# Optimization experiments

Hardware: AMD Instinct MI355X
Metric: run time of the kernel (lower is better)

The kernel has to match this reference:

```python
import jax, jax.numpy as jnp
import numpy as np

# Flattened-state gather indices. State is prev[9,3] flattened to 27 values,
# then concat with x -> flat[29], where flat[27]=a=x[0], flat[28]=b=x[1].
# Row t gives the (x0, x1, x2) inputs of triangle t, read from the source wiring.
IDX0 = np.array([3, 0, 6, 12, 9, 15, 18, 6, 15])   # x0 inputs
IDX1 = np.array([1, 7, 4, 19, 16, 13, 10, 22, 25])  # x1 inputs
IDX2 = np.array([17, 5, 11, 8, 28, 2, 27, 23, 26])  # x2 inputs (t=4 -> b, t=6 -> a)

NOISE_SCALE = 0.125  # LUT2 hard-codes noise = 0.125


def mux(s, a, b):
    return 0.5 * (s * b - s * a + a + b)


def setup_inputs() -> dict:
    key = jax.random.key(0)
    k1, k2, k3 = jax.random.split(key, 3)
    x = jax.random.normal(k1, (2,), dtype=jnp.float32)
    weights = jax.random.normal(k2, (9, 3, 4), dtype=jnp.float32)  # 9 triangles x 3 LUT2s x 4 weights
    noise = jax.random.normal(k3, (130, 9, 3, 4), dtype=jnp.float32)  # per-step np.random.normal draws
    return {"x": x, "weights": weights, "noise": noise, "dummy1": 0, "dummy2": 0}


def reference(x, weights, noise, dummy1, dummy2):
    del dummy1, dummy2  # unused in the original forward

    def step(prev, n):
        # prev: [9,3] current states; n: [9,3,4] noise for this step
        flat = jnp.concatenate([prev.reshape(-1), x])  # [29]
        x0, x1, x2 = flat[IDX0], flat[IDX1], flat[IDX2]  # each [9]
        # LUT j of each triangle: LUT0(x1,x2), LUT1(x0,x2), LUT2(x0,x1)
        A = jnp.stack([x1, x0, x0], axis=1)  # [9,3] first mux select
        B = jnp.stack([x2, x2, x1], axis=1)  # [9,3] second mux select
        w = weights + jnp.abs(1.0 - jnp.abs(weights)) * n * NOISE_SCALE  # [9,3,4]
        m0 = mux(A, w[..., 0], w[..., 1])
        m1 = mux(A, w[..., 2], w[..., 3])
        new = mux(B, m0, m1)  # [9,3] synchronous update (uupdate after all forwards)
        return new, None

    init = -jnp.ones((9, 3), dtype=x.dtype)  # all states start at -1
    final, _ = jax.lax.scan(step, init, noise)  # 130 steps
    return jnp.stack([final[0, 1], final[1, 2], final[7, 2]])
```

## Files before the change

### kernel.cpp

```cpp
#include <hip/hip_runtime.h>


#define STEPS 130
#define NLUT  27

__device__ __constant__ int c_idx0[9] = {3, 0, 6, 12, 9, 15, 18, 6, 15};
__device__ __constant__ int c_idx1[9] = {1, 7, 4, 19, 16, 13, 10, 22, 25};
__device__ __constant__ int c_idx2[9] = {17, 5, 11, 8, 28, 2, 27, 23, 26};

__global__ __launch_bounds__(1024)
void one_layer_net_kernel(const float* __restrict__ x,
                          const float* __restrict__ weights,
                          const float* __restrict__ noise,
                          float* __restrict__ out) {
    __shared__ float4 tbl[STEPS * NLUT];

    const int tid = threadIdx.x;
    const float a = x[0];
    const float b = x[1];

    const float4* __restrict__ w4 = (const float4*)weights;
    const float4* __restrict__ n4 = (const float4*)noise;
    for (int i = tid; i < STEPS * NLUT; i += 1024) {
        const int l = i % NLUT;
        float4 w = w4[l];
        float4 n = n4[i];
        float w0 = fmaf(fabsf(1.0f - fabsf(w.x)) * n.x, 0.125f, w.x);
        float w1 = fmaf(fabsf(1.0f - fabsf(w.y)) * n.y, 0.125f, w.y);
        float w2 = fmaf(fabsf(1.0f - fabsf(w.z)) * n.z, 0.125f, w.z);
        float w3 = fmaf(fabsf(1.0f - fabsf(w.w)) * n.w, 0.125f, w.w);
        float d0 = w1 - w0, s0 = w0 + w1;
        float d1 = w3 - w2, s1 = w2 + w3;
        float K3 = 0.25f * (d1 - d0);
        float K2 = 0.25f * (s1 - s0);
        float K1 = 0.25f * (d0 + d1);
        float K0 = 0.25f * (s0 + s1);
        if (l == 12 || l == 13) {
            K0 = fmaf(K2, b, K0); K1 = fmaf(K3, b, K1); K2 = 0.0f; K3 = 0.0f;
        }
        if (l == 18 || l == 19) {
            K0 = fmaf(K2, a, K0); K1 = fmaf(K3, a, K1); K2 = 0.0f; K3 = 0.0f;
        }
        tbl[i] = make_float4(K3, K2, K1, K0);
    }
    __syncthreads();

    if (tid >= 64) return;

    const int l  = tid;
    const int lc = (l < NLUT) ? l : (NLUT - 1);
    const int t  = lc / 3;
    const int j  = lc % 3;
    int srcA = (j == 0) ? c_idx1[t] : c_idx0[t];
    int srcB = (j == 2) ? c_idx1[t] : c_idx2[t];
    if (srcB >= NLUT) srcB = 0;
    const int bpA = srcA << 2;
    const int bpB = srcB << 2;

    float state = -1.0f;

    const float4* __restrict__ row = &tbl[lc];
    float4 k = row[0];
    #pragma unroll
    for (int s = 0; s < STEPS; ++s) {
        const float4 kc = k;
        if (s + 1 < STEPS) k = row[(s + 1) * NLUT];
        const int si = __float_as_int(state);
        const float gA = __int_as_float(__builtin_amdgcn_ds_bpermute(bpA, si));
        const float gB = __int_as_float(__builtin_amdgcn_ds_bpermute(bpB, si));
        const float t0 = fmaf(gA, kc.x, kc.y);
        const float t1 = fmaf(gA, kc.z, kc.w);
        state = fmaf(gB, t0, t1);
    }

    if (l == 1)  out[0] = state;
    if (l == 5)  out[1] = state;
    if (l == 23) out[2] = state;
}

extern "C" void kernel_launch(void* const* d_in, const int* in_sizes, int n_in,
                              void* d_out, int out_size, void* d_ws, size_t ws_size,
                              hipStream_t stream) {
    const float* x       = (const float*)d_in[0];
    const float* weights = (const float*)d_in[1];
    const float* noise   = (const float*)d_in[2];
    float* out = (float*)d_out;
    one_layer_net_kernel<<<1, 1024, 0, stream>>>(x, weights, noise, out);
}
```

Before: 65.37 us.

## Unroll recurrence three steps per round via composed wiring to cut bpermute latency chain

Replaces the per-step pair of cross-lane permutes with a three-step composed evaluation: each lane gathers 8 states from three hops back in the wiring graph and evaluates a tree of 7 LUT polynomials, advancing 3 steps per round (43 rounds plus one final step). This shortens the serial dependency chain of ds_bpermute latencies from 130 to 44 rounds. In exchange each round does 8 permutes and 7 LDS table loads plus redundant arithmetic. Correctness depends on the composed wiring and row offsets (steps 3r..3r+2) lining up, and on the clamped srcB=0 path for external inputs being harmless.

```diff
diff --git a/kernel.cpp b/kernel.cpp
--- a/kernel.cpp
+++ b/kernel.cpp
@@ -3,10 +3,29 @@
 
 #define STEPS 130
 #define NLUT  27
+#define ROUNDS 43
 
 __device__ __constant__ int c_idx0[9] = {3, 0, 6, 12, 9, 15, 18, 6, 15};
 __device__ __constant__ int c_idx1[9] = {1, 7, 4, 19, 16, 13, 10, 22, 25};
 __device__ __constant__ int c_idx2[9] = {17, 5, 11, 8, 28, 2, 27, 23, 26};
+
+__device__ __forceinline__ int wA(int m) {
+    int t = m / 3, j = m % 3;
+    return (j == 0) ? c_idx1[t] : c_idx0[t];
+}
+__device__ __forceinline__ int wB(int m) {
+    int t = m / 3, j = m % 3;
+    int s = (j == 2) ? c_idx1[t] : c_idx2[t];
+    return (s >= NLUT) ? 0 : s;
+}
+
+__device__ __forceinline__ float evalE(float4 k, float x, float y) {
+    return fmaf(y, fmaf(x, k.x, k.y), fmaf(x, k.z, k.w));
+}
+
+__device__ __forceinline__ float bperm(int byteIdx, float v) {
+    return __int_as_float(__builtin_amdgcn_ds_bpermute(byteIdx, __float_as_int(v)));
+}
 
 __global__ __launch_bounds__(1024)
 void one_layer_net_kernel(const float* __restrict__ x,
@@ -49,28 +68,53 @@
 
     const int l  = tid;
     const int lc = (l < NLUT) ? l : (NLUT - 1);
-    const int t  = lc / 3;
-    const int j  = lc % 3;
-    int srcA = (j == 0) ? c_idx1[t] : c_idx0[t];
-    int srcB = (j == 2) ? c_idx1[t] : c_idx2[t];
-    if (srcB >= NLUT) srcB = 0;
-    const int bpA = srcA << 2;
-    const int bpB = srcB << 2;
+
+    const int a0 = wA(lc), b0 = wB(lc);
+    const int a1 = wA(a0), b1 = wB(a0);
+    const int a2 = wA(b0), b2 = wB(b0);
+    const int g0 = wA(a1) << 2, g1 = wB(a1) << 2;
+    const int g2 = wA(b1) << 2, g3 = wB(b1) << 2;
+    const int g4 = wA(a2) << 2, g5 = wB(a2) << 2;
+    const int g6 = wA(b2) << 2, g7 = wB(b2) << 2;
+
+    const float4* __restrict__ pA1 = tbl + 0 * NLUT + a1;
+    const float4* __restrict__ pA2 = tbl + 0 * NLUT + b1;
+    const float4* __restrict__ pA3 = tbl + 0 * NLUT + a2;
+    const float4* __restrict__ pA4 = tbl + 0 * NLUT + b2;
+    const float4* __restrict__ pB1 = tbl + 1 * NLUT + a0;
+    const float4* __restrict__ pB2 = tbl + 1 * NLUT + b0;
+    const float4* __restrict__ pC  = tbl + 2 * NLUT + lc;
 
     float state = -1.0f;
 
-    const float4* __restrict__ row = &tbl[lc];
-    float4 k = row[0];
     #pragma unroll
-    for (int s = 0; s < STEPS; ++s) {
-        const float4 kc = k;
-        if (s + 1 < STEPS) k = row[(s + 1) * NLUT];
-        const int si = __float_as_int(state);
-        const float gA = __int_as_float(__builtin_amdgcn_ds_bpermute(bpA, si));
-        const float gB = __int_as_float(__builtin_amdgcn_ds_bpermute(bpB, si));
-        const float t0 = fmaf(gA, kc.x, kc.y);
-        const float t1 = fmaf(gA, kc.z, kc.w);
-        state = fmaf(gB, t0, t1);
+    for (int r = 0; r < ROUNDS; ++r) {
+        const int o = r * 3 * NLUT;
+        const float p0 = bperm(g0, state);
+        const float p1 = bperm(g1, state);
+        const float p2 = bperm(g2, state);
+        const float p3 = bperm(g3, state);
+        const float p4 = bperm(g4, state);
+        const float p5 = bperm(g5, state);
+        const float p6 = bperm(g6, state);
+        const float p7 = bperm(g7, state);
+        const float4 kA1 = pA1[o], kA2 = pA2[o], kA3 = pA3[o], kA4 = pA4[o];
+        const float4 kB1 = pB1[o], kB2 = pB2[o];
+        const float4 kC  = pC[o];
+        const float u1 = evalE(kA1, p0, p1);
+        const float u2 = evalE(kA2, p2, p3);
+        const float u3 = evalE(kA3, p4, p5);
+        const float u4 = evalE(kA4, p6, p7);
+        const float v1 = evalE(kB1, u1, u2);
+        const float v2 = evalE(kB2, u3, u4);
+        state = evalE(kC, v1, v2);
+    }
+
+    {
+        const float4 kc = tbl[(STEPS - 1) * NLUT + lc];
+        const float gA = bperm(a0 << 2, state);
+        const float gB = bperm(b0 << 2, state);
+        state = evalE(kc, gA, gB);
     }
 
     if (l == 1)  out[0] = state;
```

Measured after the change: 67.95 us. 3.9% more time.

## Advance two recurrence steps per round using two-hop neighbor gathers

Applied to the files above, without the earlier changes.

Rewrites the serial 130-step recurrence so that each iteration computes two steps. Each lane gathers the four grand-predecessor states with independent bpermutes, then evaluates the two intermediate predecessor LUTs locally. This halves the number of dependent bpermute round trips on the critical path, in exchange for more bpermutes and more table reads per round. Handling of the constant-folded a/b inputs relies on the table precomputation already in place.

```diff
diff --git a/kernel.cpp b/kernel.cpp
--- a/kernel.cpp
+++ b/kernel.cpp
@@ -3,10 +3,29 @@
 
 #define STEPS 130
 #define NLUT  27
+#define ROUNDS 65
 
 __device__ __constant__ int c_idx0[9] = {3, 0, 6, 12, 9, 15, 18, 6, 15};
 __device__ __constant__ int c_idx1[9] = {1, 7, 4, 19, 16, 13, 10, 22, 25};
 __device__ __constant__ int c_idx2[9] = {17, 5, 11, 8, 28, 2, 27, 23, 26};
+
+__device__ __forceinline__ int wA(int m) {
+    int t = m / 3, j = m % 3;
+    return (j == 0) ? c_idx1[t] : c_idx0[t];
+}
+__device__ __forceinline__ int wB(int m) {
+    int t = m / 3, j = m % 3;
+    int s = (j == 2) ? c_idx1[t] : c_idx2[t];
+    return (s >= NLUT) ? 0 : s;
+}
+
+__device__ __forceinline__ float evalE(float4 k, float x, float y) {
+    return fmaf(y, fmaf(x, k.x, k.y), fmaf(x, k.z, k.w));
+}
+
+__device__ __forceinline__ float bperm(int byteIdx, float v) {
+    return __int_as_float(__builtin_amdgcn_ds_bpermute(byteIdx, __float_as_int(v)));
+}
 
 __global__ __launch_bounds__(1024)
 void one_layer_net_kernel(const float* __restrict__ x,
@@ -49,28 +68,30 @@
 
     const int l  = tid;
     const int lc = (l < NLUT) ? l : (NLUT - 1);
-    const int t  = lc / 3;
-    const int j  = lc % 3;
-    int srcA = (j == 0) ? c_idx1[t] : c_idx0[t];
-    int srcB = (j == 2) ? c_idx1[t] : c_idx2[t];
-    if (srcB >= NLUT) srcB = 0;
-    const int bpA = srcA << 2;
-    const int bpB = srcB << 2;
+
+    const int a0 = wA(lc), b0 = wB(lc);
+    const int g0 = wA(a0) << 2, g1 = wB(a0) << 2;
+    const int g2 = wA(b0) << 2, g3 = wB(b0) << 2;
+
+    const float4* __restrict__ pA = tbl + 0 * NLUT + a0;
+    const float4* __restrict__ pB = tbl + 0 * NLUT + b0;
+    const float4* __restrict__ pC = tbl + 1 * NLUT + lc;
 
     float state = -1.0f;
 
-    const float4* __restrict__ row = &tbl[lc];
-    float4 k = row[0];
     #pragma unroll
-    for (int s = 0; s < STEPS; ++s) {
-        const float4 kc = k;
-        if (s + 1 < STEPS) k = row[(s + 1) * NLUT];
-        const int si = __float_as_int(state);
-        const float gA = __int_as_float(__builtin_amdgcn_ds_bpermute(bpA, si));
-        const float gB = __int_as_float(__builtin_amdgcn_ds_bpermute(bpB, si));
-        const float t0 = fmaf(gA, kc.x, kc.y);
-        const float t1 = fmaf(gA, kc.z, kc.w);
-        state = fmaf(gB, t0, t1);
+    for (int r = 0; r < ROUNDS; ++r) {
+        const int o = r * 2 * NLUT;
+        const float q0 = bperm(g0, state);
+        const float q1 = bperm(g1, state);
+        const float q2 = bperm(g2, state);
+        const float q3 = bperm(g3, state);
+        const float4 kA = pA[o];
+        const float4 kB = pB[o];
+        const float4 kC = pC[o];
+        const float u1 = evalE(kA, q0, q1);
+        const float u2 = evalE(kB, q2, q3);
+        state = evalE(kC, u1, u2);
     }
 
     if (l == 1)  out[0] = state;
```

Measured after the change: 64.89 us. About the same (-0.7%).
